# Kernel tuning notes

Measured on AMD Instinct MI355X. Metric: run time of the kernel, lower is better.

The kernel has to match this reference:

```python
import jax, jax.numpy as jnp
import numpy as np

N_NODES = 100000
N_EDGES = 1600000
IN_DIM, HID_DIM, OUT_DIM = 128, 256, 128


def setup_inputs() -> dict:
    key = jax.random.key(0)
    ks = jax.random.split(key, 5)
    x = jax.random.normal(ks[0], (N_NODES, IN_DIM), dtype=jnp.float32)
    src = jax.random.randint(ks[1], (N_EDGES,), 0, N_NODES, dtype=jnp.int64)
    dst = jax.random.randint(ks[2], (N_EDGES,), 0, N_NODES, dtype=jnp.int64)
    # Glorot-ish init for linear weights (DGL GraphConv default), zero bias
    W1 = jax.random.normal(ks[3], (IN_DIM, HID_DIM), dtype=jnp.float32) * (1.0 / np.sqrt(IN_DIM))
    W2 = jax.random.normal(ks[4], (HID_DIM, OUT_DIM), dtype=jnp.float32) * (1.0 / np.sqrt(HID_DIM))
    b1 = jnp.zeros((HID_DIM,), dtype=jnp.float32)
    b2 = jnp.zeros((OUT_DIM,), dtype=jnp.float32)
    return {"x": x, "src": src, "dst": dst, "W1": W1, "b1": b1, "W2": W2, "b2": b2}


def _degree_norms(src, dst, n_nodes):
    # norm='both': D_out(src)^{-1/2} on messages, D_in(dst)^{-1/2} on aggregate;
    # degrees clamped to min 1 as in DGL.
    ones = jnp.ones(src.shape[0], dtype=jnp.float32)
    deg_out = jax.ops.segment_sum(ones, src, num_segments=n_nodes)
    deg_in = jax.ops.segment_sum(ones, dst, num_segments=n_nodes)
    norm_src = jax.lax.rsqrt(jnp.maximum(deg_out, 1.0))
    norm_dst = jax.lax.rsqrt(jnp.maximum(deg_in, 1.0))
    return norm_src, norm_dst


def _graph_conv(x, src, dst, W, b, norm_src, norm_dst):
    h = x * norm_src[:, None]                                  # [N, d]
    agg = jax.ops.segment_sum(h[src], dst, num_segments=x.shape[0])  # [N, d]
    agg = agg * norm_dst[:, None]
    return agg @ W + b


def reference(x, src, dst, W1, b1, W2, b2):
    norm_src, norm_dst = _degree_norms(src, dst, x.shape[0])
    h = jax.nn.relu(_graph_conv(x, src, dst, W1, b1, norm_src, norm_dst))
    out = _graph_conv(h, src, dst, W2, b2, norm_src, norm_dst)
    return out
```

## Files before the change

### kernel.cpp

```cpp
#include <hip/hip_runtime.h>

constexpr int N_NODES = 100000;
constexpr int N_EDGES = 1600000;
constexpr int DIN = 128, DHID = 256, DOUT = 128;

constexpr int NB = 256;
constexpr int BR = 391;
constexpr int CAP = 8192;
constexpr int NBLK1 = 512;
constexpr int CHUNK = (N_EDGES + NBLK1 - 1) / NBLK1;

typedef __bf16 bf16x8 __attribute__((ext_vector_type(8)));
typedef float f32x4 __attribute__((ext_vector_type(4)));

static __device__ __forceinline__ ushort f2bf(float f) {
    uint u = __float_as_uint(f);
    uint r = (u + 0x7FFFu + ((u >> 16) & 1u)) >> 16;
    return (ushort)r;
}
static __device__ __forceinline__ float bf2f(ushort h) {
    return __uint_as_float(((uint)h) << 16);
}
static __device__ __forceinline__ float bflo(uint w) { return __uint_as_float(w << 16); }
static __device__ __forceinline__ float bfhi(uint w) { return __uint_as_float(w & 0xFFFF0000u); }

__global__ __launch_bounds__(256) void part_kernel(const int* __restrict__ src,
                                                   const int* __restrict__ dst,
                                                   int* __restrict__ curA, int* __restrict__ curB,
                                                   uint* __restrict__ ppair,
                                                   ushort* __restrict__ psv, int e,
                                                   const float* __restrict__ W1,
                                                   ushort* __restrict__ Wf1,
                                                   const float* __restrict__ W2,
                                                   ushort* __restrict__ Wf2) {
    const int t = threadIdx.x;
    if (blockIdx.x >= NBLK1) {
        int i = (blockIdx.x - NBLK1) * 256 + t;
        if (i < DIN * DHID) {
            int frag = i >> 9, r = i & 511;
            int lane = r >> 3, ee = r & 7;
            int kb = frag & 3, ii = (frag >> 2) & 1, w = (frag >> 3) & 3, kh = frag >> 5;
            int c = w * 32 + ii * 16 + (lane & 15);
            int k = kb * 32 + (lane >> 4) * 8 + ee;
            Wf1[i] = f2bf(W1[k * DHID + kh * 128 + c]);
        } else {
            int i2 = i - DIN * DHID;
            int frag = i2 >> 9, r = i2 & 511;
            int lane = r >> 3, ee = r & 7;
            int kb2 = frag & 3, j2 = (frag >> 2) & 1, w = (frag >> 3) & 3, kh = frag >> 5;
            int c2 = w * 32 + j2 * 16 + (lane & 15);
            int k2 = kh * 128 + kb2 * 32 + (lane >> 4) * 8 + ee;
            Wf2[i2] = f2bf(W2[k2 * DOUT + c2]);
        }
        return;
    }
    __shared__ uint2 estage[CHUNK];
    __shared__ int hA[NB], hB[NB], rA[NB], rB[NB], cA[NB], cB[NB];
    const int b0 = blockIdx.x * CHUNK;
    const int cnt = min(e - b0, CHUNK);
    hA[t] = 0; hB[t] = 0; cA[t] = 0; cB[t] = 0;
    __syncthreads();
    for (int i = t; i < cnt; i += 256) {
        int s = src[b0 + i], d = dst[b0 + i];
        estage[i] = make_uint2((uint)d, (uint)s);
        atomicAdd(&hA[d / BR], 1);
        atomicAdd(&hB[s / BR], 1);
    }
    __syncthreads();
    rA[t] = atomicAdd(&curA[t], hA[t]);
    rB[t] = atomicAdd(&curB[t], hB[t]);
    __syncthreads();
    for (int i = t; i < cnt; i += 256) {
        uint2 ed = estage[i];
        int d = (int)ed.x, s = (int)ed.y;
        int bd = d / BR;
        int bs = s / BR;
        int p = rA[bd] + atomicAdd(&cA[bd], 1);
        if (p < CAP) ppair[(size_t)bd * CAP + p] = ((uint)(d - bd * BR) << 17) | (uint)s;
        int q = rB[bs] + atomicAdd(&cB[bs], 1);
        if (q < CAP) psv[(size_t)bs * CAP + q] = (ushort)(s - bs * BR);
    }
}

__global__ __launch_bounds__(512) void csrn_kernel(const int* __restrict__ curA,
                                                   const int* __restrict__ curB,
                                                   const uint* __restrict__ ppair,
                                                   const ushort* __restrict__ psv,
                                                   int* __restrict__ csr,
                                                   int* __restrict__ rowstart,
                                                   float* __restrict__ ndst,
                                                   float* __restrict__ nsrc,
                                                   const float* __restrict__ x,
                                                   ushort* __restrict__ xb, int n, int e) {
    __shared__ uint ploc[CAP];
    __shared__ int hist[512], sc[512], exc[512], cur[512];
    __shared__ int sbst;
    const int t = threadIdx.x;
    const int b = blockIdx.x;
    const int first = b * BR;
    const int nr = min(BR, n - first);
    const int cntA = min(curA[b], CAP);
    const size_t base = (size_t)b * CAP;

    if (t < 256) sc[t] = curA[t];
    __syncthreads();
    for (int off = 1; off < 256; off <<= 1) {
        int add = 0;
        if (t < 256 && t >= off) add = sc[t - off];
        __syncthreads();
        if (t < 256) sc[t] += add;
        __syncthreads();
    }
    if (t == 0) {
        sbst = (b == 0) ? 0 : sc[b - 1];
        if (b == 0) rowstart[n] = e;
    }
    hist[t] = 0;
    cur[t] = 0;
    __syncthreads();
    const int bst = sbst;

    for (int i = t; i < cntA; i += 512) {
        uint p = ppair[base + i];
        ploc[i] = p;
        atomicAdd(&hist[p >> 17], 1);
    }
    __syncthreads();
    int h = hist[t];
    sc[t] = h;
    __syncthreads();
    for (int off = 1; off < 512; off <<= 1) {
        int add = (t >= off) ? sc[t - off] : 0;
        __syncthreads();
        sc[t] += add;
        __syncthreads();
    }
    exc[t] = sc[t] - h;
    if (t < nr) {
        rowstart[first + t] = bst + exc[t];
        ndst[first + t] = rsqrtf(fmaxf((float)h, 1.0f));
    }
    __syncthreads();
    for (int i = t; i < cntA; i += 512) {
        uint p = ploc[i];
        int dl = p >> 17;
        int pos = exc[dl] + atomicAdd(&cur[dl], 1);
        csr[bst + pos] = (int)(p & 0x1FFFFu);
    }

    __syncthreads();
    hist[t] = 0;
    __syncthreads();
    const int cntB = min(curB[b], CAP);
    for (int i = t; i < cntB; i += 512) atomicAdd(&hist[psv[base + i]], 1);
    __syncthreads();
    float* nsv = (float*)exc;
    if (t < nr) {
        float v = rsqrtf(fmaxf((float)hist[t], 1.0f));
        nsrc[first + t] = v;
        nsv[t] = v;
    }
    __syncthreads();

    const int rl = t >> 5, q = t & 31;
    for (int i = rl; i < nr; i += 16) {
        float s = nsv[i];
        const size_t ro = (size_t)(first + i) * 128;
        float4 v = *(const float4*)&x[ro + q * 4];
        ushort4 o = {f2bf(v.x * s), f2bf(v.y * s), f2bf(v.z * s), f2bf(v.w * s)};
        *(ushort4*)&xb[ro + q * 4] = o;
    }
}

template <bool OUTBF16, bool ADDBIAS>
__global__ __launch_bounds__(256) void aggh_kernel(const ushort* __restrict__ Xb,
                                                   const int* __restrict__ csr,
                                                   const int* __restrict__ rowstart,
                                                   const float* __restrict__ ndst,
                                                   const float* __restrict__ bias,
                                                   float* __restrict__ outf,
                                                   ushort* __restrict__ outb, int n, int half) {
    int g = threadIdx.x >> 3;
    int lane = threadIdx.x & 7;
    int d = blockIdx.x * 32 + g;
    if (d >= n) return;
    int beg = rowstart[d], end = rowstart[d + 1];
    const int fo = half * 64 + lane * 8;
    const ushort* Xp = Xb + fo;
    float acc[8];
#pragma unroll
    for (int j = 0; j < 8; j++) acc[j] = 0.f;

#define ACC8(v)                                   \
    do {                                          \
        acc[0] += bflo(v.x); acc[1] += bfhi(v.x); \
        acc[2] += bflo(v.y); acc[3] += bfhi(v.y); \
        acc[4] += bflo(v.z); acc[5] += bfhi(v.z); \
        acc[6] += bflo(v.w); acc[7] += bfhi(v.w); \
    } while (0)

    int k = beg;
    for (; k + 4 <= end; k += 4) {
        int s0 = csr[k], s1 = csr[k + 1], s2 = csr[k + 2], s3 = csr[k + 3];
        uint4 v0 = *(const uint4*)(Xp + (size_t)s0 * 128);
        uint4 v1 = *(const uint4*)(Xp + (size_t)s1 * 128);
        uint4 v2 = *(const uint4*)(Xp + (size_t)s2 * 128);
        uint4 v3 = *(const uint4*)(Xp + (size_t)s3 * 128);
        ACC8(v0);
        ACC8(v1);
        ACC8(v2);
        ACC8(v3);
    }
    for (; k < end; ++k) {
        uint4 v = *(const uint4*)(Xp + (size_t)csr[k] * 128);
        ACC8(v);
    }
#undef ACC8

    float nd = ndst[d];
#pragma unroll
    for (int j = 0; j < 8; j++) acc[j] *= nd;
    if constexpr (ADDBIAS) {
        float4 b0 = *(const float4*)&bias[fo];
        float4 b1 = *(const float4*)&bias[fo + 4];
        acc[0] += b0.x; acc[1] += b0.y; acc[2] += b0.z; acc[3] += b0.w;
        acc[4] += b1.x; acc[5] += b1.y; acc[6] += b1.z; acc[7] += b1.w;
    }
    if constexpr (OUTBF16) {
        uint4 o;
        o.x = (uint)f2bf(acc[0]) | ((uint)f2bf(acc[1]) << 16);
        o.y = (uint)f2bf(acc[2]) | ((uint)f2bf(acc[3]) << 16);
        o.z = (uint)f2bf(acc[4]) | ((uint)f2bf(acc[5]) << 16);
        o.w = (uint)f2bf(acc[6]) | ((uint)f2bf(acc[7]) << 16);
        *(uint4*)(outb + (size_t)d * 128 + fo) = o;
    } else {
        float4 o0 = {acc[0], acc[1], acc[2], acc[3]};
        float4 o1 = {acc[4], acc[5], acc[6], acc[7]};
        *(float4*)(outf + (size_t)d * 128 + fo) = o0;
        *(float4*)(outf + (size_t)d * 128 + fo + 4) = o1;
    }
}

__global__ __launch_bounds__(256) void fused64_kernel(const ushort* __restrict__ A,
                                                      const ushort* __restrict__ Wf1,
                                                      const float* __restrict__ b1,
                                                      const float* __restrict__ nsrc,
                                                      const ushort* __restrict__ Wf2,
                                                      ushort* __restrict__ T, int M) {
    __shared__ ushort Sa[64][128];
    __shared__ ushort H1[64][128];
    const int row0 = blockIdx.x * 64;
    const int t = threadIdx.x;
    const int w = t >> 6, lane = t & 63;
    const int l16 = lane & 15, lk = lane >> 4;

    float nsv[4];
#pragma unroll
    for (int j = 0; j < 4; j++) {
        int gm = row0 + j * 16 + l16;
        nsv[j] = nsrc[gm < M ? gm : (M - 1)];
    }
    float4 bvv[2][2];
#pragma unroll
    for (int kh = 0; kh < 2; kh++)
#pragma unroll
        for (int i = 0; i < 2; i++)
            bvv[kh][i] = *(const float4*)&b1[kh * 128 + w * 32 + i * 16 + lk * 4];

#pragma unroll
    for (int i = 0; i < 4; i++) {
        int idx = i * 256 + t;
        int r = idx >> 4, oct = idx & 15;
        int gr = row0 + r;
        uint4 v = make_uint4(0u, 0u, 0u, 0u);
        if (gr < M) v = *(const uint4*)&A[(size_t)gr * 128 + oct * 8];
        *(uint4*)((char*)&Sa[0][0] + r * 256 + (oct ^ (r & 15)) * 16) = v;
    }
    __syncthreads();

    f32x4 acc2[4][2];
#pragma unroll
    for (int i = 0; i < 4; i++)
#pragma unroll
        for (int j = 0; j < 2; j++) acc2[i][j] = (f32x4){0.f, 0.f, 0.f, 0.f};

    for (int kh = 0; kh < 2; kh++) {
        const ushort* w1p = Wf1 + ((size_t)(kh * 4 + w) * 8) * 512 + lane * 8;
        const ushort* w2p = Wf2 + ((size_t)(kh * 4 + w) * 8) * 512 + lane * 8;
        bf16x8 af[2][4], wb[2][4];
#pragma unroll
        for (int i = 0; i < 2; i++)
#pragma unroll
            for (int kb = 0; kb < 4; kb++) af[i][kb] = *(const bf16x8*)(w1p + (i * 4 + kb) * 512);
#pragma unroll
        for (int j2 = 0; j2 < 2; j2++)
#pragma unroll
            for (int kb2 = 0; kb2 < 4; kb2++)
                wb[j2][kb2] = *(const bf16x8*)(w2p + (j2 * 4 + kb2) * 512);

        f32x4 acc1[2][4];
#pragma unroll
        for (int i = 0; i < 2; i++)
#pragma unroll
            for (int j = 0; j < 4; j++) acc1[i][j] = (f32x4){0.f, 0.f, 0.f, 0.f};

#pragma unroll
        for (int kb = 0; kb < 4; kb++) {
            bf16x8 bf_[4];
#pragma unroll
            for (int j = 0; j < 4; j++) {
                int m = j * 16 + l16;
                bf_[j] = *(const bf16x8*)((const char*)&Sa[0][0] + m * 256 +
                                          ((kb * 4 + lk) ^ l16) * 16);
            }
#pragma unroll
            for (int i = 0; i < 2; i++)
#pragma unroll
                for (int j = 0; j < 4; j++)
                    acc1[i][j] =
                        __builtin_amdgcn_mfma_f32_16x16x32_bf16(af[i][kb], bf_[j], acc1[i][j], 0, 0, 0);
        }
        __syncthreads();

#pragma unroll
        for (int i = 0; i < 2; i++) {
            int cb = w * 32 + i * 16 + lk * 4;
            float4 bv = bvv[kh][i];
#pragma unroll
            for (int j = 0; j < 4; j++) {
                int m = j * 16 + l16;
                float ns = nsv[j];
                ushort4 pk;
                pk.x = f2bf(fmaxf(acc1[i][j][0] + bv.x, 0.f) * ns);
                pk.y = f2bf(fmaxf(acc1[i][j][1] + bv.y, 0.f) * ns);
                pk.z = f2bf(fmaxf(acc1[i][j][2] + bv.z, 0.f) * ns);
                pk.w = f2bf(fmaxf(acc1[i][j][3] + bv.w, 0.f) * ns);
                int oct = cb >> 3;
                *(ushort4*)((char*)&H1[0][0] + m * 256 + ((oct ^ l16) & 15) * 16 +
                            (cb & 7) * 2) = pk;
            }
        }
        __syncthreads();

#pragma unroll
        for (int kb2 = 0; kb2 < 4; kb2++) {
            bf16x8 ha[4];
#pragma unroll
            for (int i2 = 0; i2 < 4; i2++) {
                int m = i2 * 16 + l16;
                ha[i2] = *(const bf16x8*)((const char*)&H1[0][0] + m * 256 +
                                          ((kb2 * 4 + lk) ^ l16) * 16);
            }
#pragma unroll
            for (int i2 = 0; i2 < 4; i2++)
#pragma unroll
                for (int j2 = 0; j2 < 2; j2++)
                    acc2[i2][j2] = __builtin_amdgcn_mfma_f32_16x16x32_bf16(ha[i2], wb[j2][kb2],
                                                                           acc2[i2][j2], 0, 0, 0);
        }
    }

#pragma unroll
    for (int i2 = 0; i2 < 4; i2++) {
#pragma unroll
        for (int j2 = 0; j2 < 2; j2++) {
#pragma unroll
            for (int q = 0; q < 4; q++) {
                int r = row0 + i2 * 16 + lk * 4 + q;
                int c = w * 32 + j2 * 16 + l16;
                if (r < M) T[(size_t)r * DOUT + c] = f2bf(acc2[i2][j2][q]);
            }
        }
    }
}

extern "C" void kernel_launch(void* const* d_in, const int* in_sizes, int n_in,
                              void* d_out, int out_size, void* d_ws, size_t ws_size,
                              hipStream_t stream) {
    const float* x  = (const float*)d_in[0];
    const int*   src = (const int*)d_in[1];
    const int*   dst = (const int*)d_in[2];
    const float* W1 = (const float*)d_in[3];
    const float* b1 = (const float*)d_in[4];
    const float* W2 = (const float*)d_in[5];
    const float* b2 = (const float*)d_in[6];
    float* out = (float*)d_out;

    const int N = N_NODES, E = N_EDGES;

    size_t off = 0;
    auto carve = [&](size_t bytes) -> void* {
        void* p = (char*)d_ws + off;
        off += (bytes + 255) & ~(size_t)255;
        return p;
    };
    int* curA     = (int*)carve(NB * 4);
    int* curB     = (int*)carve(NB * 4);
    int* rowstart = (int*)carve((size_t)(N + 1) * 4);
    float* ndst   = (float*)carve((size_t)N * 4);
    float* nsrc   = (float*)carve((size_t)N * 4);
    int* csr      = (int*)carve((size_t)E * 4);
    ushort* Wf1   = (ushort*)carve(DIN * DHID * 2);
    ushort* Wf2   = (ushort*)carve(DHID * DOUT * 2);
    ushort* xb    = (ushort*)carve((size_t)N * DIN * 2);
    ushort* agg1b = (ushort*)carve((size_t)N * DIN * 2);
    ushort* tb    = (ushort*)carve((size_t)N * DOUT * 2);
    uint*   ppair = (uint*)carve((size_t)NB * CAP * 4);
    ushort* psv   = (ushort*)carve((size_t)NB * CAP * 2);

    hipMemsetAsync(curA, 0, 2 * NB * 4, stream);

    part_kernel<<<NBLK1 + 256, 256, 0, stream>>>(src, dst, curA, curB, ppair, psv, E,
                                                 W1, Wf1, W2, Wf2);
    csrn_kernel<<<NB, 512, 0, stream>>>(curA, curB, ppair, psv, csr, rowstart, ndst, nsrc,
                                        x, xb, N, E);

    const int gagg = (N + 31) / 32;
    aggh_kernel<true, false><<<gagg, 256, 0, stream>>>(xb, csr, rowstart, ndst, nullptr,
                                                       nullptr, agg1b, N, 0);
    aggh_kernel<true, false><<<gagg, 256, 0, stream>>>(xb, csr, rowstart, ndst, nullptr,
                                                       nullptr, agg1b, N, 1);

    fused64_kernel<<<(N + 63) / 64, 256, 0, stream>>>(agg1b, Wf1, b1, nsrc, Wf2, tb, N);

    aggh_kernel<false, true><<<gagg, 256, 0, stream>>>(tb, csr, rowstart, ndst, b2,
                                                       out, nullptr, N, 0);
    aggh_kernel<false, true><<<gagg, 256, 0, stream>>>(tb, csr, rowstart, ndst, b2,
                                                       out, nullptr, N, 1);
}
```

Measured before the change: 217.1 us.

## Double bucket count, sort CSR rows by source, split x conversion kernel

Halves the node range per partition bucket (512 buckets of 196 rows), so the CSR build runs on twice as many blocks with smaller shared-memory staging. Each destination row's source list is insertion-sorted in shared memory before being written out, which should make the neighbour gathers in aggregation more cache-friendly. The scaled bf16 conversion of x moves out of the CSR kernel into its own fully parallel kernel. This adds one launch and per-row serial sorting work, and lowers the per-bucket capacity to 4096, which leaves less headroom against overflow.

```diff
diff --git a/kernel.cpp b/kernel.cpp
--- a/kernel.cpp
+++ b/kernel.cpp
@@ -4,9 +4,9 @@
 constexpr int N_EDGES = 1600000;
 constexpr int DIN = 128, DHID = 256, DOUT = 128;
 
-constexpr int NB = 256;
-constexpr int BR = 391;
-constexpr int CAP = 8192;
+constexpr int NB2 = 512;
+constexpr int BR2 = 196;
+constexpr int CAP2 = 4096;
 constexpr int NBLK1 = 512;
 constexpr int CHUNK = (N_EDGES + NBLK1 - 1) / NBLK1;
 
@@ -55,30 +55,32 @@
         return;
     }
     __shared__ uint2 estage[CHUNK];
-    __shared__ int hA[NB], hB[NB], rA[NB], rB[NB], cA[NB], cB[NB];
+    __shared__ int hA[NB2], hB[NB2], rA[NB2], rB[NB2], cA[NB2], cB[NB2];
     const int b0 = blockIdx.x * CHUNK;
     const int cnt = min(e - b0, CHUNK);
-    hA[t] = 0; hB[t] = 0; cA[t] = 0; cB[t] = 0;
+    for (int j = t; j < NB2; j += 256) { hA[j] = 0; hB[j] = 0; cA[j] = 0; cB[j] = 0; }
     __syncthreads();
     for (int i = t; i < cnt; i += 256) {
         int s = src[b0 + i], d = dst[b0 + i];
         estage[i] = make_uint2((uint)d, (uint)s);
-        atomicAdd(&hA[d / BR], 1);
-        atomicAdd(&hB[s / BR], 1);
-    }
-    __syncthreads();
-    rA[t] = atomicAdd(&curA[t], hA[t]);
-    rB[t] = atomicAdd(&curB[t], hB[t]);
+        atomicAdd(&hA[d / BR2], 1);
+        atomicAdd(&hB[s / BR2], 1);
+    }
+    __syncthreads();
+    for (int j = t; j < NB2; j += 256) {
+        rA[j] = atomicAdd(&curA[j], hA[j]);
+        rB[j] = atomicAdd(&curB[j], hB[j]);
+    }
     __syncthreads();
     for (int i = t; i < cnt; i += 256) {
         uint2 ed = estage[i];
         int d = (int)ed.x, s = (int)ed.y;
-        int bd = d / BR;
-        int bs = s / BR;
+        int bd = d / BR2;
+        int bs = s / BR2;
         int p = rA[bd] + atomicAdd(&cA[bd], 1);
-        if (p < CAP) ppair[(size_t)bd * CAP + p] = ((uint)(d - bd * BR) << 17) | (uint)s;
+        if (p < CAP2) ppair[(size_t)bd * CAP2 + p] = ((uint)(d - bd * BR2) << 17) | (uint)s;
         int q = rB[bs] + atomicAdd(&cB[bs], 1);
-        if (q < CAP) psv[(size_t)bs * CAP + q] = (ushort)(s - bs * BR);
+        if (q < CAP2) psv[(size_t)bs * CAP2 + q] = (ushort)(s - bs * BR2);
     }
 }
 
@@ -89,26 +91,24 @@
                                                    int* __restrict__ csr,
                                                    int* __restrict__ rowstart,
                                                    float* __restrict__ ndst,
-                                                   float* __restrict__ nsrc,
-                                                   const float* __restrict__ x,
-                                                   ushort* __restrict__ xb, int n, int e) {
-    __shared__ uint ploc[CAP];
-    __shared__ int hist[512], sc[512], exc[512], cur[512];
+                                                   float* __restrict__ nsrc, int n, int e) {
+    __shared__ uint ploc[CAP2];
+    __shared__ int cloc[CAP2];
+    __shared__ int hist[NB2], sc[NB2], exc[NB2], cur[NB2];
     __shared__ int sbst;
     const int t = threadIdx.x;
     const int b = blockIdx.x;
-    const int first = b * BR;
-    const int nr = min(BR, n - first);
-    const int cntA = min(curA[b], CAP);
-    const size_t base = (size_t)b * CAP;
-
-    if (t < 256) sc[t] = curA[t];
-    __syncthreads();
-    for (int off = 1; off < 256; off <<= 1) {
-        int add = 0;
-        if (t < 256 && t >= off) add = sc[t - off];
-        __syncthreads();
-        if (t < 256) sc[t] += add;
+    const int first = b * BR2;
+    const int nr = min(BR2, n - first);
+    const int cntA = min(curA[b], CAP2);
+    const size_t base = (size_t)b * CAP2;
+
+    sc[t] = curA[t];
+    __syncthreads();
+    for (int off = 1; off < 512; off <<= 1) {
+        int add = (t >= off) ? sc[t - off] : 0;
+        __syncthreads();
+        sc[t] += add;
         __syncthreads();
     }
     if (t == 0) {
@@ -145,31 +145,43 @@
         uint p = ploc[i];
         int dl = p >> 17;
         int pos = exc[dl] + atomicAdd(&cur[dl], 1);
-        csr[bst + pos] = (int)(p & 0x1FFFFu);
-    }
+        cloc[pos] = (int)(p & 0x1FFFFu);
+    }
+    __syncthreads();
+    for (int r = t; r < nr; r += 512) {
+        int s0 = exc[r], len = hist[r];
+        for (int a = 1; a < len; a++) {
+            int v = cloc[s0 + a];
+            int bp = s0 + a;
+            while (bp > s0 && cloc[bp - 1] > v) {
+                cloc[bp] = cloc[bp - 1];
+                bp--;
+            }
+            cloc[bp] = v;
+        }
+    }
+    __syncthreads();
+    for (int i = t; i < cntA; i += 512) csr[bst + i] = cloc[i];
 
     __syncthreads();
     hist[t] = 0;
     __syncthreads();
-    const int cntB = min(curB[b], CAP);
+    const int cntB = min(curB[b], CAP2);
     for (int i = t; i < cntB; i += 512) atomicAdd(&hist[psv[base + i]], 1);
     __syncthreads();
-    float* nsv = (float*)exc;
-    if (t < nr) {
-        float v = rsqrtf(fmaxf((float)hist[t], 1.0f));
-        nsrc[first + t] = v;
-        nsv[t] = v;
-    }
-    __syncthreads();
-
-    const int rl = t >> 5, q = t & 31;
-    for (int i = rl; i < nr; i += 16) {
-        float s = nsv[i];
-        const size_t ro = (size_t)(first + i) * 128;
-        float4 v = *(const float4*)&x[ro + q * 4];
-        ushort4 o = {f2bf(v.x * s), f2bf(v.y * s), f2bf(v.z * s), f2bf(v.w * s)};
-        *(ushort4*)&xb[ro + q * 4] = o;
-    }
+    if (t < nr) nsrc[first + t] = rsqrtf(fmaxf((float)hist[t], 1.0f));
+}
+
+__global__ __launch_bounds__(256) void xbconv_kernel(const float* __restrict__ x,
+                                                     const float* __restrict__ nsrc,
+                                                     ushort* __restrict__ xb, int n) {
+    int i = blockIdx.x * 256 + threadIdx.x;
+    if (i >= n * 32) return;
+    int row = i >> 5;
+    float s = nsrc[row];
+    float4 v = *(const float4*)&x[(size_t)i * 4];
+    ushort4 o = {f2bf(v.x * s), f2bf(v.y * s), f2bf(v.z * s), f2bf(v.w * s)};
+    *(ushort4*)&xb[(size_t)i * 4] = o;
 }
 
 template <bool OUTBF16, bool ADDBIAS>
@@ -394,8 +406,8 @@
         off += (bytes + 255) & ~(size_t)255;
         return p;
     };
-    int* curA     = (int*)carve(NB * 4);
-    int* curB     = (int*)carve(NB * 4);
+    int* curA     = (int*)carve(NB2 * 4);
+    int* curB     = (int*)carve(NB2 * 4);
     int* rowstart = (int*)carve((size_t)(N + 1) * 4);
     float* ndst   = (float*)carve((size_t)N * 4);
     float* nsrc   = (float*)carve((size_t)N * 4);
@@ -405,15 +417,16 @@
     ushort* xb    = (ushort*)carve((size_t)N * DIN * 2);
     ushort* agg1b = (ushort*)carve((size_t)N * DIN * 2);
     ushort* tb    = (ushort*)carve((size_t)N * DOUT * 2);
-    uint*   ppair = (uint*)carve((size_t)NB * CAP * 4);
-    ushort* psv   = (ushort*)carve((size_t)NB * CAP * 2);
-
-    hipMemsetAsync(curA, 0, 2 * NB * 4, stream);
+    uint*   ppair = (uint*)carve((size_t)NB2 * CAP2 * 4);
+    ushort* psv   = (ushort*)carve((size_t)NB2 * CAP2 * 2);
+
+    hipMemsetAsync(curA, 0, 2 * NB2 * 4, stream);
 
     part_kernel<<<NBLK1 + 256, 256, 0, stream>>>(src, dst, curA, curB, ppair, psv, E,
                                                  W1, Wf1, W2, Wf2);
-    csrn_kernel<<<NB, 512, 0, stream>>>(curA, curB, ppair, psv, csr, rowstart, ndst, nsrc,
-                                        x, xb, N, E);
+    csrn_kernel<<<NB2, 512, 0, stream>>>(curA, curB, ppair, psv, csr, rowstart, ndst, nsrc,
+                                         N, E);
+    xbconv_kernel<<<(N * 32 + 255) / 256, 256, 0, stream>>>(x, nsrc, xb, N);
 
     const int gagg = (N + 31) / 32;
     aggh_kernel<true, false><<<gagg, 256, 0, stream>>>(xb, csr, rowstart, ndst, nullptr,
```

Measured after the change: 251.3 us. +15.8%, slower.
